# Performance work log

Hardware: AMD Instinct MI355X
Metric: run time of the kernel (lower is better)

The kernel has to match this reference:

```python
import jax, jax.numpy as jnp
import numpy as np

N_NODES = 100000
N_EDGES = 1600000
DIMS = [128, 128, 128, 128]  # in -> l0 -> l1 -> l2
BN_EPS = 1e-5


def setup_inputs() -> dict:
    key = jax.random.key(0)
    ks = jax.random.split(key, 16)
    inp = {
        "x": jax.random.normal(ks[0], (N_NODES, DIMS[0]), dtype=jnp.float32),
        "edge_index": jax.random.randint(ks[1], (2, N_EDGES), 0, N_NODES, dtype=jnp.int64),
    }
    for i in range(3):
        fan_in, fan_out = DIMS[i], DIMS[i + 1]
        scale = 1.0 / np.sqrt(fan_in)
        inp[f"W{i}"] = jax.random.uniform(ks[2 + 4 * i], (fan_in, fan_out), minval=-scale, maxval=scale, dtype=jnp.float32)
        inp[f"b{i}"] = jnp.zeros((fan_out,), dtype=jnp.float32)
        inp[f"gamma{i}"] = jnp.ones((fan_out,), dtype=jnp.float32)
        inp[f"beta{i}"] = jnp.zeros((fan_out,), dtype=jnp.float32)
    return inp


def _gcn_conv(h, src, dst, dinv_sqrt, W, b):
    # PyG GCNConv: x@W, then symmetric-normalized aggregation with self-loops, then +bias
    hw = h @ W  # [N, out]
    norm = dinv_sqrt[src] * dinv_sqrt[dst]  # [E]
    agg = jax.ops.segment_sum(hw[src] * norm[:, None], dst, num_segments=N_NODES)
    agg = agg + hw * (dinv_sqrt * dinv_sqrt)[:, None]  # self-loop contribution (weight 1/deg)
    return agg + b


def _bn(h, gamma, beta):
    mean = jnp.mean(h, axis=0)
    var = jnp.mean(jnp.square(h - mean), axis=0)  # biased var, as torch BN uses for normalization
    return gamma * (h - mean) * jax.lax.rsqrt(var + BN_EPS) + beta


def reference(x, edge_index, W0, b0, gamma0, beta0, W1, b1, gamma1, beta1, W2, b2, gamma2, beta2):
    src, dst = edge_index[0], edge_index[1]
    # degree with self-loops (edge weight 1), computed once; same adjacency each layer
    deg = jax.ops.segment_sum(jnp.ones((N_EDGES,), dtype=x.dtype), dst, num_segments=N_NODES) + 1.0
    dinv_sqrt = jax.lax.rsqrt(deg)
    h = x
    for W, b, g, be in ((W0, b0, gamma0, beta0), (W1, b1, gamma1, beta1), (W2, b2, gamma2, beta2)):
        h = _gcn_conv(h, src, dst, dinv_sqrt, W, b)
        h = _bn(h, g, be)
        h = jax.nn.relu(h)
    return h
```

## Files before the change

### kernel.cpp

```cpp
#include <hip/hip_runtime.h>
#include <hip/hip_bf16.h>

#define NN 100000
#define NE 1600000
#define BN_EPS 1e-5f
#define NB 391

typedef __attribute__((ext_vector_type(8))) short bf16x8;
typedef __attribute__((ext_vector_type(4))) float f32x4;

static __device__ __forceinline__ ushort f2b(float f) {
  __hip_bfloat16 h = __float2bfloat16(f);
  return __builtin_bit_cast(ushort, h);
}
static __device__ __forceinline__ float blo(uint v) { return __builtin_bit_cast(float, v << 16); }
static __device__ __forceinline__ float bhi(uint v) { return __builtin_bit_cast(float, v & 0xFFFF0000u); }

__global__ __launch_bounds__(256) void k_count(const int* __restrict__ ei, int* __restrict__ deg) {
  int e = blockIdx.x * 256 + threadIdx.x;
  atomicAdd(&deg[ei[NE + e]], 1);
}

__global__ __launch_bounds__(256) void k_dinv(const int* __restrict__ deg, float* __restrict__ dinv) {
  int v = blockIdx.x * 256 + threadIdx.x;
  if (v < NN) dinv[v] = rsqrtf((float)deg[v] + 1.0f);
}

__global__ __launch_bounds__(256) void k_scan1(const int* __restrict__ deg, int* __restrict__ bsum) {
  __shared__ int lds[256];
  const int t = threadIdx.x;
  const int i = blockIdx.x * 256 + t;
  lds[t] = (i < NN) ? deg[i] : 0;
  __syncthreads();
  for (int d = 128; d > 0; d >>= 1) {
    if (t < d) lds[t] += lds[t + d];
    __syncthreads();
  }
  if (t == 0) bsum[blockIdx.x] = lds[0];
}

__global__ __launch_bounds__(512) void k_scan2(const int* __restrict__ bsum, int* __restrict__ boff,
                                               int* __restrict__ rp) {
  __shared__ int lds[512];
  const int t = threadIdx.x;
  const int own = (t < NB) ? bsum[t] : 0;
  lds[t] = own;
  __syncthreads();
  for (int d = 1; d < 512; d <<= 1) {
    int v = (t >= d) ? lds[t - d] : 0;
    __syncthreads();
    lds[t] += v;
    __syncthreads();
  }
  if (t < NB) boff[t] = lds[t] - own;
  if (t == 511) rp[NN] = lds[511];
}

__global__ __launch_bounds__(256) void k_scan3(const int* __restrict__ deg, const int* __restrict__ boff,
                                               int* __restrict__ rp) {
  __shared__ int lds[256];
  const int t = threadIdx.x;
  const int i = blockIdx.x * 256 + t;
  const int own = (i < NN) ? deg[i] : 0;
  lds[t] = own;
  __syncthreads();
  for (int d = 1; d < 256; d <<= 1) {
    int v = (t >= d) ? lds[t - d] : 0;
    __syncthreads();
    lds[t] += v;
    __syncthreads();
  }
  if (i < NN) rp[i] = boff[blockIdx.x] + lds[t] - own;
}

__global__ __launch_bounds__(256) void k_scatter(const int* __restrict__ ei, const int* __restrict__ rp,
                                                 int* __restrict__ fill, int* __restrict__ csr) {
  int e = blockIdx.x * 256 + threadIdx.x;
  int d = ei[NE + e];
  int pos = rp[d] + atomicAdd(&fill[d], 1);
  csr[pos] = ei[e];
}

__global__ __launch_bounds__(128) void k_wt(const float* __restrict__ W0, const float* __restrict__ W1,
                                            const float* __restrict__ W2, ushort* __restrict__ wt) {
  const int lay = blockIdx.y, n = blockIdx.x, k = threadIdx.x;
  const float* W = (lay == 0) ? W0 : (lay == 1) ? W1 : W2;
  wt[lay * 16384 + n * 128 + k] = f2b(W[k * 128 + n]);
}

__global__ __launch_bounds__(256) void k_tobf(const float* __restrict__ x, ushort* __restrict__ o) {
  int i = blockIdx.x * 256 + threadIdx.x;
  float4 v = ((const float4*)x)[i];
  ushort4 u;
  u.x = f2b(v.x); u.y = f2b(v.y); u.z = f2b(v.z); u.w = f2b(v.w);
  ((ushort4*)o)[i] = u;
}

__global__ __launch_bounds__(256) void k_gemm(const ushort* __restrict__ h,
                                              const ushort* __restrict__ wt,
                                              ushort* __restrict__ hw) {
  __shared__ ushort wlds[128 * 128];
  const int t = threadIdx.x;
  {
    const uint4* src = (const uint4*)wt;
    uint4* dst = (uint4*)wlds;
    #pragma unroll
    for (int i = 0; i < 8; ++i) {
      int idx = t + i * 256;
      int n = idx >> 4;
      dst[idx ^ (n & 7)] = src[idx];
    }
  }
  __syncthreads();

  const int wv = t >> 6, l = t & 63;
  const int lr = l & 15, lk = l >> 4;
  const int row0 = blockIdx.x * 128 + wv * 32;
  f32x4 acc[2][8] = {};
  const uint4* wchunks = (const uint4*)wlds;

  #pragma unroll
  for (int kb = 0; kb < 4; ++kb) {
    const int r0 = min(row0 + lr, NN - 1);
    const int r1 = min(row0 + 16 + lr, NN - 1);
    const bf16x8 a0 = *(const bf16x8*)(h + (size_t)r0 * 128 + kb * 32 + lk * 8);
    const bf16x8 a1 = *(const bf16x8*)(h + (size_t)r1 * 128 + kb * 32 + lk * 8);
    #pragma unroll
    for (int nt = 0; nt < 8; ++nt) {
      const int n = nt * 16 + lr;
      const int chunk = n * 16 + ((kb * 4 + lk) ^ (n & 7));
      const bf16x8 b = *(const bf16x8*)(wchunks + chunk);
      acc[0][nt] = __builtin_amdgcn_mfma_f32_16x16x32_bf16(a0, b, acc[0][nt], 0, 0, 0);
      acc[1][nt] = __builtin_amdgcn_mfma_f32_16x16x32_bf16(a1, b, acc[1][nt], 0, 0, 0);
    }
  }
  #pragma unroll
  for (int rt = 0; rt < 2; ++rt)
    #pragma unroll
    for (int j = 0; j < 4; ++j) {
      const int row = row0 + rt * 16 + lk * 4 + j;
      if (row < NN) {
        #pragma unroll
        for (int nt = 0; nt < 8; ++nt)
          hw[(size_t)row * 128 + nt * 16 + lr] = f2b(acc[rt][nt][j]);
      }
    }
}

__global__ __launch_bounds__(256) void k_agg(const ushort* __restrict__ hw,
                                             const int* __restrict__ rp, const int* __restrict__ csr,
                                             const float* __restrict__ dinv, const float* __restrict__ bias,
                                             float* __restrict__ out) {
  const int wid = (blockIdx.x * 256 + threadIdx.x) >> 6;
  const int lane = threadIdx.x & 63;
  if (wid >= NN) return;
  const int v = wid;
  const int beg = rp[v], end = rp[v + 1];
  float ax = 0.f, ay = 0.f;
  int i = beg;
  for (; i + 4 <= end; i += 4) {
    const int s0 = csr[i], s1 = csr[i + 1], s2 = csr[i + 2], s3 = csr[i + 3];
    const float d0 = dinv[s0], d1 = dinv[s1], d2 = dinv[s2], d3 = dinv[s3];
    const uint v0 = *(const uint*)(hw + (size_t)s0 * 128 + 2 * lane);
    const uint v1 = *(const uint*)(hw + (size_t)s1 * 128 + 2 * lane);
    const uint v2 = *(const uint*)(hw + (size_t)s2 * 128 + 2 * lane);
    const uint v3 = *(const uint*)(hw + (size_t)s3 * 128 + 2 * lane);
    ax = fmaf(d0, blo(v0), ax); ay = fmaf(d0, bhi(v0), ay);
    ax = fmaf(d1, blo(v1), ax); ay = fmaf(d1, bhi(v1), ay);
    ax = fmaf(d2, blo(v2), ax); ay = fmaf(d2, bhi(v2), ay);
    ax = fmaf(d3, blo(v3), ax); ay = fmaf(d3, bhi(v3), ay);
  }
  for (; i < end; ++i) {
    const int s = csr[i];
    const float ds = dinv[s];
    const uint vv = *(const uint*)(hw + (size_t)s * 128 + 2 * lane);
    ax = fmaf(ds, blo(vv), ax); ay = fmaf(ds, bhi(vv), ay);
  }
  const float dv = dinv[v];
  const uint sv = *(const uint*)(hw + (size_t)v * 128 + 2 * lane);
  const float bx = bias[2 * lane], by = bias[2 * lane + 1];
  float2 o;
  o.x = fmaf(ax, dv, fmaf(blo(sv), dv * dv, bx));
  o.y = fmaf(ay, dv, fmaf(bhi(sv), dv * dv, by));
  *(float2*)(out + (size_t)v * 128 + 2 * lane) = o;
}

__global__ __launch_bounds__(256) void k_bnstats(const float* __restrict__ h, float* __restrict__ stats) {
  __shared__ float rs[256], rs2[256];
  const int t = threadIdx.x;
  const int col = t & 127, rg = t >> 7;
  const int row0 = blockIdx.x * 128;
  const int rend = min(row0 + 128, NN);
  float s = 0.f, s2 = 0.f;
  for (int r = row0 + rg; r < rend; r += 2) {
    float v = h[(size_t)r * 128 + col];
    s += v;
    s2 = fmaf(v, v, s2);
  }
  rs[t] = s; rs2[t] = s2;
  __syncthreads();
  if (t < 128) {
    atomicAdd(&stats[t], rs[t] + rs[t + 128]);
    atomicAdd(&stats[128 + t], rs2[t] + rs2[t + 128]);
  }
}

__global__ void k_bnfin(const float* __restrict__ stats, const float* __restrict__ gamma,
                        const float* __restrict__ beta, float* __restrict__ sc, float* __restrict__ sh) {
  const int c = threadIdx.x;
  const float inv_n = 1.0f / (float)NN;
  const float mean = stats[c] * inv_n;
  const float var = fmaxf(stats[128 + c] * inv_n - mean * mean, 0.f);
  const float k = gamma[c] * rsqrtf(var + BN_EPS);
  sc[c] = k;
  sh[c] = fmaf(-mean, k, beta[c]);
}

__global__ __launch_bounds__(256) void k_bnrelu(const float* __restrict__ h, ushort* __restrict__ ob,
                                                float* __restrict__ of, const int write_f32,
                                                const float* __restrict__ sc, const float* __restrict__ sh) {
  const int i = blockIdx.x * 256 + threadIdx.x;
  const int c = (i & 31) * 4;
  float4 v = ((const float4*)h)[i];
  v.x = fmaxf(fmaf(sc[c + 0], v.x, sh[c + 0]), 0.f);
  v.y = fmaxf(fmaf(sc[c + 1], v.y, sh[c + 1]), 0.f);
  v.z = fmaxf(fmaf(sc[c + 2], v.z, sh[c + 2]), 0.f);
  v.w = fmaxf(fmaf(sc[c + 3], v.w, sh[c + 3]), 0.f);
  ushort4 u;
  u.x = f2b(v.x); u.y = f2b(v.y); u.z = f2b(v.z); u.w = f2b(v.w);
  ((ushort4*)ob)[i] = u;
  if (write_f32) ((float4*)of)[i] = v;
}

extern "C" void kernel_launch(void* const* d_in, const int* in_sizes, int n_in,
                              void* d_out, int out_size, void* d_ws, size_t ws_size,
                              hipStream_t stream) {
  const float* x  = (const float*)d_in[0];
  const int*   ei = (const int*)d_in[1];
  const float* W[3]  = {(const float*)d_in[2],  (const float*)d_in[6],  (const float*)d_in[10]};
  const float* b[3]  = {(const float*)d_in[3],  (const float*)d_in[7],  (const float*)d_in[11]};
  const float* g[3]  = {(const float*)d_in[4],  (const float*)d_in[8],  (const float*)d_in[12]};
  const float* be[3] = {(const float*)d_in[5],  (const float*)d_in[9],  (const float*)d_in[13]};

  char* ws = (char*)d_ws;
  ushort* hwb   = (ushort*)(ws);
  ushort* hin   = (ushort*)(ws + 25600000);
  int*    csr   = (int*)(ws + 51200000);
  int*    deg   = (int*)(ws + 57600000);
  int*    rp    = (int*)(ws + 58000000);
  int*    fill  = (int*)(ws + 58400016);
  float*  dinv  = (float*)(ws + 58800016);
  ushort* wtb   = (ushort*)(ws + 59200016);
  float*  stats = (float*)(ws + 59298320);
  float*  sc    = (float*)(ws + 59299344);
  float*  sh    = (float*)(ws + 59299856);
  int*    bsum  = (int*)(ws + 59300368);
  int*    boff  = (int*)(ws + 59301936);
  float*  hbuf  = (float*)d_out;

  hipMemsetAsync(deg, 0, NN * 4, stream);
  hipMemsetAsync(fill, 0, NN * 4, stream);
  k_count<<<NE / 256, 256, 0, stream>>>(ei, deg);
  k_dinv<<<(NN + 255) / 256, 256, 0, stream>>>(deg, dinv);
  k_scan1<<<NB, 256, 0, stream>>>(deg, bsum);
  k_scan2<<<1, 512, 0, stream>>>(bsum, boff, rp);
  k_scan3<<<NB, 256, 0, stream>>>(deg, boff, rp);
  k_scatter<<<NE / 256, 256, 0, stream>>>(ei, rp, fill, csr);
  k_wt<<<dim3(128, 3), 128, 0, stream>>>(W[0], W[1], W[2], wtb);
  k_tobf<<<NN * 128 / 1024, 256, 0, stream>>>(x, hin);

  for (int L = 0; L < 3; ++L) {
    k_gemm<<<(NN + 127) / 128, 256, 0, stream>>>(hin, wtb + L * 16384, hwb);
    k_agg<<<25000, 256, 0, stream>>>(hwb, rp, csr, dinv, b[L], hbuf);
    hipMemsetAsync(stats, 0, 256 * 4, stream);
    k_bnstats<<<(NN + 127) / 128, 256, 0, stream>>>(hbuf, stats);
    k_bnfin<<<1, 128, 0, stream>>>(stats, g[L], be[L], sc, sh);
    k_bnrelu<<<NN * 128 / 1024, 256, 0, stream>>>(hbuf, hin, hbuf, (L == 2) ? 1 : 0, sc, sh);
  }
}
```

Before: 764.5 us.

## Bucket edges for CSR build and restructure aggregation into column-sliced 8-lane groups

CSR construction now bins edges into per-128-node buckets (eight slices per bucket) in the same pass that counts degrees. A per-bucket kernel then scatters into the CSR using shared-memory atomics instead of global atomics on a fill array. The aggregation kernel is reorganized so each block handles 32 nodes in one 16-column slice: 8 lanes cooperatively load eight neighbor indices and broadcast them with shuffles, using nontemporal loads and stores. The fixed bucket capacity of 512 assumes about 256 edges per bucket for uniform random edges and would overflow on skewed degree distributions. Each node's edge list is now read eight times, once per column slice, in exchange for better locality on the gather.

Result: slower. 1.340 ms (+75.3%).

```diff
diff --git a/kernel.cpp b/kernel.cpp
--- a/kernel.cpp
+++ b/kernel.cpp
@@ -5,9 +5,12 @@
 #define NE 1600000
 #define BN_EPS 1e-5f
 #define NB 391
+#define NBKT 782
+#define BCAP 512
 
 typedef __attribute__((ext_vector_type(8))) short bf16x8;
 typedef __attribute__((ext_vector_type(4))) float f32x4;
+typedef __attribute__((ext_vector_type(2))) float f32x2;
 
 static __device__ __forceinline__ ushort f2b(float f) {
   __hip_bfloat16 h = __float2bfloat16(f);
@@ -16,9 +19,16 @@
 static __device__ __forceinline__ float blo(uint v) { return __builtin_bit_cast(float, v << 16); }
 static __device__ __forceinline__ float bhi(uint v) { return __builtin_bit_cast(float, v & 0xFFFF0000u); }
 
-__global__ __launch_bounds__(256) void k_count(const int* __restrict__ ei, int* __restrict__ deg) {
-  int e = blockIdx.x * 256 + threadIdx.x;
-  atomicAdd(&deg[ei[NE + e]], 1);
+__global__ __launch_bounds__(256) void k_bin(const int* __restrict__ ei, int* __restrict__ deg,
+                                             int* __restrict__ bfill, uint* __restrict__ binned) {
+  const int e = blockIdx.x * 256 + threadIdx.x;
+  const int s = ei[e];
+  const int d = ei[NE + e];
+  atomicAdd(&deg[d], 1);
+  const int bucket = d >> 7;
+  const int idx = (blockIdx.x & 7) * NBKT + bucket;
+  const int pos = atomicAdd(&bfill[idx], 1);
+  binned[(size_t)idx * BCAP + pos] = ((uint)(d & 127) << 17) | (uint)s;
 }
 
 __global__ __launch_bounds__(256) void k_dinv(const int* __restrict__ deg, float* __restrict__ dinv) {
@@ -73,12 +83,32 @@
   if (i < NN) rp[i] = boff[blockIdx.x] + lds[t] - own;
 }
 
-__global__ __launch_bounds__(256) void k_scatter(const int* __restrict__ ei, const int* __restrict__ rp,
-                                                 int* __restrict__ fill, int* __restrict__ csr) {
-  int e = blockIdx.x * 256 + threadIdx.x;
-  int d = ei[NE + e];
-  int pos = rp[d] + atomicAdd(&fill[d], 1);
-  csr[pos] = ei[e];
+__global__ __launch_bounds__(256) void k_scatter2(const uint* __restrict__ binned,
+                                                  const int* __restrict__ bfill,
+                                                  const int* __restrict__ rp, int* __restrict__ csr) {
+  __shared__ int lfill[128];
+  __shared__ int lrp[128];
+  const int t = threadIdx.x;
+  const int bucket = blockIdx.x;
+  const int v0 = bucket << 7;
+  if (t < 128) {
+    lfill[t] = 0;
+    lrp[t] = (v0 + t < NN) ? rp[v0 + t] : 0;
+  }
+  __syncthreads();
+  #pragma unroll
+  for (int r = 0; r < 8; ++r) {
+    const int idx = r * NBKT + bucket;
+    const int c = bfill[idx];
+    const uint* seg = binned + (size_t)idx * BCAP;
+    for (int j = t; j < c; j += 256) {
+      const uint u = seg[j];
+      const int ld = u >> 17;
+      const int s = (int)(u & 0x1FFFFu);
+      const int pos = lrp[ld] + atomicAdd(&lfill[ld], 1);
+      csr[pos] = s;
+    }
+  }
 }
 
 __global__ __launch_bounds__(128) void k_wt(const float* __restrict__ W0, const float* __restrict__ W1,
@@ -151,38 +181,41 @@
                                              const int* __restrict__ rp, const int* __restrict__ csr,
                                              const float* __restrict__ dinv, const float* __restrict__ bias,
                                              float* __restrict__ out) {
-  const int wid = (blockIdx.x * 256 + threadIdx.x) >> 6;
-  const int lane = threadIdx.x & 63;
-  if (wid >= NN) return;
-  const int v = wid;
+  const int slice = blockIdx.x & 7;
+  const int ng = blockIdx.x >> 3;
+  const int g = threadIdx.x >> 3;
+  const int sub = threadIdx.x & 7;
+  const int v = ng * 32 + g;
   const int beg = rp[v], end = rp[v + 1];
+  const size_t coff = (size_t)slice * 16 + sub * 2;
   float ax = 0.f, ay = 0.f;
   int i = beg;
-  for (; i + 4 <= end; i += 4) {
-    const int s0 = csr[i], s1 = csr[i + 1], s2 = csr[i + 2], s3 = csr[i + 3];
-    const float d0 = dinv[s0], d1 = dinv[s1], d2 = dinv[s2], d3 = dinv[s3];
-    const uint v0 = *(const uint*)(hw + (size_t)s0 * 128 + 2 * lane);
-    const uint v1 = *(const uint*)(hw + (size_t)s1 * 128 + 2 * lane);
-    const uint v2 = *(const uint*)(hw + (size_t)s2 * 128 + 2 * lane);
-    const uint v3 = *(const uint*)(hw + (size_t)s3 * 128 + 2 * lane);
-    ax = fmaf(d0, blo(v0), ax); ay = fmaf(d0, bhi(v0), ay);
-    ax = fmaf(d1, blo(v1), ax); ay = fmaf(d1, bhi(v1), ay);
-    ax = fmaf(d2, blo(v2), ax); ay = fmaf(d2, bhi(v2), ay);
-    ax = fmaf(d3, blo(v3), ax); ay = fmaf(d3, bhi(v3), ay);
+  for (; i + 8 <= end; i += 8) {
+    const int e = __builtin_nontemporal_load(csr + i + sub);
+    const float dn = dinv[e];
+    #pragma unroll
+    for (int j = 0; j < 8; ++j) {
+      const int s = __shfl(e, j, 8);
+      const float dj = __shfl(dn, j, 8);
+      const uint vv = *(const uint*)(hw + (size_t)s * 128 + coff);
+      ax = fmaf(dj, blo(vv), ax);
+      ay = fmaf(dj, bhi(vv), ay);
+    }
   }
   for (; i < end; ++i) {
-    const int s = csr[i];
+    const int s = __builtin_nontemporal_load(csr + i);
     const float ds = dinv[s];
-    const uint vv = *(const uint*)(hw + (size_t)s * 128 + 2 * lane);
-    ax = fmaf(ds, blo(vv), ax); ay = fmaf(ds, bhi(vv), ay);
+    const uint vv = *(const uint*)(hw + (size_t)s * 128 + coff);
+    ax = fmaf(ds, blo(vv), ax);
+    ay = fmaf(ds, bhi(vv), ay);
   }
   const float dv = dinv[v];
-  const uint sv = *(const uint*)(hw + (size_t)v * 128 + 2 * lane);
-  const float bx = bias[2 * lane], by = bias[2 * lane + 1];
-  float2 o;
-  o.x = fmaf(ax, dv, fmaf(blo(sv), dv * dv, bx));
-  o.y = fmaf(ay, dv, fmaf(bhi(sv), dv * dv, by));
-  *(float2*)(out + (size_t)v * 128 + 2 * lane) = o;
+  const uint sv = *(const uint*)(hw + (size_t)v * 128 + coff);
+  const f32x2 bb = *(const f32x2*)(bias + slice * 16 + sub * 2);
+  f32x2 o;
+  o.x = fmaf(ax, dv, fmaf(blo(sv), dv * dv, bb.x));
+  o.y = fmaf(ay, dv, fmaf(bhi(sv), dv * dv, bb.y));
+  __builtin_nontemporal_store(o, (f32x2*)(out + (size_t)v * 128 + slice * 16 + sub * 2));
 }
 
 __global__ __launch_bounds__(256) void k_bnstats(const float* __restrict__ h, float* __restrict__ stats) {
@@ -244,28 +277,29 @@
 
   char* ws = (char*)d_ws;
   ushort* hwb   = (ushort*)(ws);
+  uint*   binned = (uint*)(ws);
+  int*    bfill  = (int*)(ws + 13000000);
   ushort* hin   = (ushort*)(ws + 25600000);
   int*    csr   = (int*)(ws + 51200000);
   int*    deg   = (int*)(ws + 57600000);
   int*    rp    = (int*)(ws + 58000000);
-  int*    fill  = (int*)(ws + 58400016);
-  float*  dinv  = (float*)(ws + 58800016);
-  ushort* wtb   = (ushort*)(ws + 59200016);
-  float*  stats = (float*)(ws + 59298320);
-  float*  sc    = (float*)(ws + 59299344);
-  float*  sh    = (float*)(ws + 59299856);
-  int*    bsum  = (int*)(ws + 59300368);
-  int*    boff  = (int*)(ws + 59301936);
+  float*  dinv  = (float*)(ws + 58400016);
+  ushort* wtb   = (ushort*)(ws + 58800016);
+  float*  stats = (float*)(ws + 58898320);
+  float*  sc    = (float*)(ws + 58899344);
+  float*  sh    = (float*)(ws + 58899856);
+  int*    bsum  = (int*)(ws + 58900368);
+  int*    boff  = (int*)(ws + 58901936);
   float*  hbuf  = (float*)d_out;
 
   hipMemsetAsync(deg, 0, NN * 4, stream);
-  hipMemsetAsync(fill, 0, NN * 4, stream);
-  k_count<<<NE / 256, 256, 0, stream>>>(ei, deg);
+  hipMemsetAsync(bfill, 0, 8 * NBKT * 4, stream);
+  k_bin<<<NE / 256, 256, 0, stream>>>(ei, deg, bfill, binned);
   k_dinv<<<(NN + 255) / 256, 256, 0, stream>>>(deg, dinv);
   k_scan1<<<NB, 256, 0, stream>>>(deg, bsum);
   k_scan2<<<1, 512, 0, stream>>>(bsum, boff, rp);
   k_scan3<<<NB, 256, 0, stream>>>(deg, boff, rp);
-  k_scatter<<<NE / 256, 256, 0, stream>>>(ei, rp, fill, csr);
+  k_scatter2<<<NBKT, 256, 0, stream>>>(binned, bfill, rp, csr);
   k_wt<<<dim3(128, 3), 128, 0, stream>>>(W[0], W[1], W[2], wtb);
   k_tobf<<<NN * 128 / 1024, 256, 0, stream>>>(x, hin);
 
```
